# Optimization experiments

Measured on AMD Instinct MI355X. Metric: run time of the kernel, lower is better.

## Reference

```python
import jax, jax.numpy as jnp
import numpy as np

B, CIN, COUT, H0 = 2, 256, 256, 128
GN_G = 16

def hsig(x):
    return jnp.clip(x + 3.0, 0.0, 6.0) / 6.0

def conv3x3(x, w, b):
    y = jax.lax.conv_general_dilated(x, w, (1, 1), ((1, 1), (1, 1)),
                                     dimension_numbers=('NCHW', 'OIHW', 'NCHW'))
    return y + b[None, :, None, None]

def group_norm(x, gamma, beta):
    Bn, C, H, W = x.shape
    xr = x.reshape(Bn, GN_G, C // GN_G, H, W)
    m = xr.mean((2, 3, 4), keepdims=True)
    v = xr.var((2, 3, 4), keepdims=True)
    xn = ((xr - m) * jax.lax.rsqrt(v + 1e-5)).reshape(Bn, C, H, W)
    return xn * gamma[None, :, None, None] + beta[None, :, None, None]

def mdconv(x, offset, mask, weight, stride):
    # Modulated deformable conv v2, 3x3 kernel, padding=1, zero-pad bilinear sampling.
    Bn, C, H, W = x.shape
    K2 = mask.shape[1]  # 9 kernel taps
    Ho, Wo = mask.shape[2], mask.shape[3]
    off = offset.reshape(Bn, K2, 2, Ho, Wo)  # (dy, dx) per tap (mmcv channel order)
    ki = jnp.arange(K2)
    py = (jnp.arange(Ho, dtype=x.dtype) * stride - 1.0)[None, None, :, None] \
         + (ki // 3).astype(x.dtype)[None, :, None, None] + off[:, :, 0]
    px = (jnp.arange(Wo, dtype=x.dtype) * stride - 1.0)[None, None, None, :] \
         + (ki % 3).astype(x.dtype)[None, :, None, None] + off[:, :, 1]
    y0f = jnp.floor(py); x0f = jnp.floor(px)
    wy = py - y0f; wx = px - x0f
    y0 = y0f.astype(jnp.int32); x0 = x0f.astype(jnp.int32)
    xf = x.reshape(Bn, C, H * W)

    def gather(yy, xx):
        valid = ((yy >= 0) & (yy < H) & (xx >= 0) & (xx < W)).astype(x.dtype)
        idx = jnp.clip(yy, 0, H - 1) * W + jnp.clip(xx, 0, W - 1)
        g = jax.vmap(lambda f, i: f[:, i])(xf, idx.reshape(Bn, -1))
        return g.reshape(Bn, C, K2, Ho, Wo) * valid[:, None]

    val = (gather(y0, x0) * ((1 - wy) * (1 - wx))[:, None]
           + gather(y0, x0 + 1) * ((1 - wy) * wx)[:, None]
           + gather(y0 + 1, x0) * (wy * (1 - wx))[:, None]
           + gather(y0 + 1, x0 + 1) * (wy * wx)[:, None])
    val = val * mask[:, None]
    return jnp.einsum('bckhw,ock->bohw', val, weight.reshape(weight.shape[0], C, K2))

def scale_attn(f, w, b):
    p = f.mean((2, 3))                  # global avg pool -> (B, C)
    s = hsig(jax.nn.relu(p @ w.T + b))  # (B, 1)
    return s[:, :, None, None]

def dyrelu(x, w1, b1, w2, b2):
    Bn, C = x.shape[0], x.shape[1]
    p = x.mean((2, 3))
    h = jax.nn.relu(p @ w1.T + b1)
    c = (hsig(h @ w2.T + b2) - 0.5).reshape(Bn, 4, C)  # a1, b1, a2, b2
    e = lambda t: t[:, :, None, None]
    a1 = c[:, 0] * 2.0 + 1.0
    a2 = c[:, 2] * 2.0
    return jnp.maximum(x * e(a1) + e(c[:, 1]), x * e(a2) + e(c[:, 3]))

def resize_align(x, Ho, Wo):
    # bilinear resize, align_corners=True
    Bn, C, H, W = x.shape
    sy = jnp.arange(Ho, dtype=x.dtype) * ((H - 1) / (Ho - 1))
    sx = jnp.arange(Wo, dtype=x.dtype) * ((W - 1) / (Wo - 1))
    yl = jnp.floor(sy).astype(jnp.int32); yh = jnp.minimum(yl + 1, H - 1)
    xl = jnp.floor(sx).astype(jnp.int32); xh = jnp.minimum(xl + 1, W - 1)
    wy = (sy - yl)[None, None, :, None]
    wx = (sx - xl)[None, None, None, :]
    t = x[:, :, yl, :] * (1 - wy) + x[:, :, yh, :] * wy
    return t[:, :, :, xl] * (1 - wx) + t[:, :, :, xh] * wx

def _forward(x0, x1, x2, w_off, b_off, w_mid, g_mid, be_mid, w_low, g_low, be_low,
             w_high, g_high, be_high, w_sa, b_sa, w_dy1, b_dy1, w_dy2, b_dy2):
    xs = [x0, x1, x2]
    L = len(xs)
    outs = []
    for l in range(L):
        om = conv3x3(xs[l], w_off, b_off)
        offset = om[:, :18]
        mask = jax.nn.sigmoid(om[:, 18:])
        mid = group_norm(mdconv(xs[l], offset, mask, w_mid, 1), g_mid, be_mid)
        sum_feat = mid * scale_attn(mid, w_sa, b_sa)
        n = 1
        if l > 0:
            low = group_norm(mdconv(xs[l - 1], offset, mask, w_low, 2), g_low, be_low)
            sum_feat = sum_feat + low * scale_attn(low, w_sa, b_sa)
            n += 1
        if l < L - 1:
            # x[l+1] has half resolution; subsample offset/mask to its grid
            o2 = offset[:, :, ::2, ::2]
            m2 = mask[:, :, ::2, ::2]
            high = group_norm(mdconv(xs[l + 1], o2, m2, w_high, 1), g_high, be_high)
            high = resize_align(high, xs[l].shape[2], xs[l].shape[3])
            sum_feat = sum_feat + high * scale_attn(high, w_sa, b_sa)
            n += 1
        outs.append(dyrelu(sum_feat / n, w_dy1, b_dy1, w_dy2, b_dy2))
    return tuple(outs)

def setup_inputs():
    key = jax.random.key(0)
    ks = jax.random.split(key, 20)
    f32 = jnp.float32
    rn = lambda k, s: jax.random.normal(k, s, f32)
    return {
        'x0': rn(ks[0], (B, CIN, H0, H0)),
        'x1': rn(ks[1], (B, CIN, H0 // 2, H0 // 2)),
        'x2': rn(ks[2], (B, CIN, H0 // 4, H0 // 4)),
        'w_off': 0.01 * rn(ks[3], (27, CIN, 3, 3)),
        'b_off': jnp.zeros((27,), f32),
        'w_mid': 0.05 * rn(ks[4], (COUT, CIN, 3, 3)),
        'g_mid': 1.0 + 0.1 * rn(ks[5], (COUT,)),
        'be_mid': 0.1 * rn(ks[6], (COUT,)),
        'w_low': 0.05 * rn(ks[7], (COUT, CIN, 3, 3)),
        'g_low': 1.0 + 0.1 * rn(ks[8], (COUT,)),
        'be_low': 0.1 * rn(ks[9], (COUT,)),
        'w_high': 0.05 * rn(ks[10], (COUT, CIN, 3, 3)),
        'g_high': 1.0 + 0.1 * rn(ks[11], (COUT,)),
        'be_high': 0.1 * rn(ks[12], (COUT,)),
        'w_sa': 0.05 * rn(ks[13], (1, COUT)),
        'b_sa': jnp.zeros((1,), f32),
        'w_dy1': 0.05 * rn(ks[14], (COUT // 4, COUT)),
        'b_dy1': jnp.zeros((COUT // 4,), f32),
        'w_dy2': 0.05 * rn(ks[15], (4 * COUT, COUT // 4)),
        'b_dy2': jnp.zeros((4 * COUT,), f32),
    }

def reference(x0, x1, x2, w_off, b_off, w_mid, g_mid, be_mid, w_low, g_low, be_low,
              w_high, g_high, be_high, w_sa, b_sa, w_dy1, b_dy1, w_dy2, b_dy2):
    return _forward(x0, x1, x2, w_off, b_off, w_mid, g_mid, be_mid, w_low, g_low,
                    be_low, w_high, g_high, be_high, w_sa, b_sa, w_dy1, b_dy1,
                    w_dy2, b_dy2)
```

## Files before the change

kernel.cpp:

```cpp
#include <hip/hip_runtime.h>
#include <hip/hip_bf16.h>
#include <math.h>

#define CIN 256
#define COUT 256
#define NB 2
#define GN_GROUPS 16

typedef __attribute__((ext_vector_type(8))) short short8;
typedef __attribute__((ext_vector_type(4))) float floatx4;

__device__ __forceinline__ float b2f(unsigned short u) {
  union { unsigned int i; float f; } v;
  v.i = ((unsigned int)u) << 16;
  return v.f;
}
__device__ __forceinline__ unsigned short f2b(float f) {
  union { float f; unsigned int i; } v;
  v.f = f;
  unsigned int r = (v.i + 0x7FFFu + ((v.i >> 16) & 1u)) >> 16;
  return (unsigned short)r;
}
__device__ __forceinline__ float lo2f(unsigned int u) {
  union { unsigned int i; float f; } v;
  v.i = u << 16;
  return v.f;
}
__device__ __forceinline__ float hi2f(unsigned int u) {
  union { unsigned int i; float f; } v;
  v.i = u & 0xffff0000u;
  return v.f;
}
__device__ __forceinline__ unsigned int pk2(float a, float b) {
  union { __hip_bfloat162 h; unsigned int u; } v;
  v.h = __float22bfloat162_rn(float2{a, b});
  return v.u;
}

struct TrB {
  const float* x0; const float* x1; const float* x2;
  unsigned short *t0, *t1, *t2, *l0, *l1, *l2;
};

__global__ __launch_bounds__(256) void transpose_kernel(TrB A) {
  __shared__ float tile[64][65];
  int bx = blockIdx.x;
  int li = (bx >= 256 ? 1 : 0) + (bx >= 320 ? 1 : 0);
  int local = bx - (li == 0 ? 0 : (li == 1 ? 256 : 320));
  const float* x = li == 0 ? A.x0 : (li == 1 ? A.x1 : A.x2);
  unsigned short* xT = li == 0 ? A.t0 : (li == 1 ? A.t1 : A.t2);
  unsigned short* xLo = li == 0 ? A.l0 : (li == 1 ? A.l1 : A.l2);
  int P = li == 0 ? 16384 : (li == 1 ? 4096 : 1024);

  int pBase = local * 64, cBase = blockIdx.y * 64, b = blockIdx.z;
  int t = threadIdx.x;
  int pl = t & 63, ch = t >> 6;
  const float* xb = x + ((size_t)b * CIN + cBase) * P + pBase;
#pragma unroll
  for (int e = 0; e < 16; e++) {
    int c = ch * 16 + e;
    tile[c][pl] = xb[(size_t)c * P + pl];
  }
  __syncthreads();
  size_t obase = ((size_t)b * P + pBase) * CIN + cBase;
  int cl = t & 63, pr = t >> 6;
#pragma unroll
  for (int e = 0; e < 16; e++) {
    int p = pr * 16 + e;
    float v = tile[cl][p];
    unsigned short h = f2b(v);
    xT[obase + (size_t)p * CIN + cl] = h;
    xLo[obase + (size_t)p * CIN + cl] = f2b(v - b2f(h));
  }
}

__global__ void repack_w_kernel(const float* __restrict__ w0,
                                const float* __restrict__ w1,
                                const float* __restrict__ w2,
                                unsigned short* __restrict__ t0,
                                unsigned short* __restrict__ t1,
                                unsigned short* __restrict__ t2) {
  int bx = blockIdx.x;
  int sel = (bx >= 2304 ? 1 : 0) + (bx >= 4608 ? 1 : 0);
  const float* w = sel == 0 ? w0 : (sel == 1 ? w1 : w2);
  unsigned short* wt = sel == 0 ? t0 : (sel == 1 ? t1 : t2);
  int idx = (bx - sel * 2304) * 256 + threadIdx.x;
  int e = idx & 7;
  int lane = (idx >> 3) & 63;
  int i = (idx >> 9) & 3;
  int wv = (idx >> 11) & 3;
  int kc = idx >> 13;
  int oc = wv * 64 + i * 16 + (lane & 15);
  int c = (kc & 7) * 32 + (lane >> 4) * 8 + e;
  int tap = kc >> 3;
  wt[idx] = f2b(w[(size_t)oc * 2304 + c * 9 + tap]);
}

__global__ void repack_wo_kernel(const float* __restrict__ w,
                                 unsigned short* __restrict__ wo) {
  int idx = blockIdx.x * 256 + threadIdx.x;
  int sel = idx / 73728;
  int r = idx % 73728;
  int k = r / 8192;
  int r2 = r % 8192;
  int cbk = r2 / 1024;
  int oc = (r2 / 32) % 32;
  int ch = r2 % 32;
  int c = cbk * 32 + ch;
  float val = (oc < 27) ? w[(size_t)oc * 2304 + c * 9 + k] : 0.0f;
  float hi = b2f(f2b(val));
  wo[idx] = sel ? f2b(val - hi) : f2b(val);
}

struct CoL {
  const unsigned short* xhi;
  const unsigned short* xlo;
  float* om;
  int H, W, Cs, cshift, Rs, P;
};
struct CoB { CoL L[3]; int off[4]; };

__global__ __launch_bounds__(256) void conv_offset_kernel(
    CoB B, const unsigned short* __restrict__ wo,
    const float* __restrict__ bias) {
  __shared__ unsigned short s_hi[204 * 40];
  __shared__ unsigned short s_lo[204 * 40];
  int bx = blockIdx.x;
  int li = (bx >= B.off[1] ? 1 : 0) + (bx >= B.off[2] ? 1 : 0);
  CoL L = B.L[li];
  int local = bx - B.off[li];
  int tpb = L.P / 64;
  int b = local / tpb, pxt = local % tpb;
  int t = threadIdx.x;
  int pbase = pxt * 64;
  int r0 = pbase / L.W;
  int c0 = pbase % L.W;
  int Ct = L.Cs + 2;
  int Npos = Ct * (L.Rs + 2);
  const unsigned short* xhib = L.xhi + (size_t)b * L.P * CIN;
  const unsigned short* xlob = L.xlo + (size_t)b * L.P * CIN;

  int lane = t & 63, wv = t >> 6, quad = lane >> 4, ln = lane & 15;
  int pl = wv * 16 + ln;
  int pi_ = pl >> L.cshift;
  int pj_ = pl & (L.Cs - 1);

  floatx4 acc0 = {0.f, 0.f, 0.f, 0.f}, acc1 = {0.f, 0.f, 0.f, 0.f};

  for (int cb = 0; cb < 8; cb++) {
    __syncthreads();
    for (int e = t; e < Npos * 4; e += 256) {
      int pos = e >> 2, oct = e & 3;
      int r = pos / Ct, c = pos % Ct;
      int gy = r0 - 1 + r, gx = c0 - 1 + c;
      uint4 vhi = {0, 0, 0, 0}, vlo = {0, 0, 0, 0};
      if (gy >= 0 && gy < L.H && gx >= 0 && gx < L.W) {
        size_t off = ((size_t)(gy * L.W + gx)) * CIN + cb * 32 + oct * 8;
        vhi = *(const uint4*)(xhib + off);
        vlo = *(const uint4*)(xlob + off);
      }
      *(uint4*)&s_hi[pos * 40 + oct * 8] = vhi;
      *(uint4*)&s_lo[pos * 40 + oct * 8] = vlo;
    }
    __syncthreads();
#pragma unroll
    for (int tap = 0; tap < 9; tap++) {
      int dy = tap / 3 - 1, dx = tap % 3 - 1;
      const unsigned short* wb0 = wo + (size_t)((0 * 9 + tap) * 8 + cb) * 1024;
      const unsigned short* wb1 = wo + (size_t)((1 * 9 + tap) * 8 + cb) * 1024;
      short8 whi0 = *(const short8*)(wb0 + ln * 32 + quad * 8);
      short8 whi1 = *(const short8*)(wb0 + (16 + ln) * 32 + quad * 8);
      short8 wlo0 = *(const short8*)(wb1 + ln * 32 + quad * 8);
      short8 wlo1 = *(const short8*)(wb1 + (16 + ln) * 32 + quad * 8);
      int pos = (pi_ + dy + 1) * Ct + (pj_ + dx + 1);
      short8 bhi = *(const short8*)&s_hi[pos * 40 + quad * 8];
      short8 blo = *(const short8*)&s_lo[pos * 40 + quad * 8];
      acc0 = __builtin_amdgcn_mfma_f32_16x16x32_bf16(whi0, bhi, acc0, 0, 0, 0);
      acc1 = __builtin_amdgcn_mfma_f32_16x16x32_bf16(whi1, bhi, acc1, 0, 0, 0);
      acc0 = __builtin_amdgcn_mfma_f32_16x16x32_bf16(wlo0, bhi, acc0, 0, 0, 0);
      acc1 = __builtin_amdgcn_mfma_f32_16x16x32_bf16(wlo1, bhi, acc1, 0, 0, 0);
      acc0 = __builtin_amdgcn_mfma_f32_16x16x32_bf16(whi0, blo, acc0, 0, 0, 0);
      acc1 = __builtin_amdgcn_mfma_f32_16x16x32_bf16(whi1, blo, acc1, 0, 0, 0);
    }
  }

  int px = pbase + pl;
#pragma unroll
  for (int i2 = 0; i2 < 2; i2++) {
#pragma unroll
    for (int r = 0; r < 4; r++) {
      int oc = i2 * 16 + quad * 4 + r;
      if (oc < 27) {
        float val = (i2 == 0 ? acc0[r] : acc1[r]) + bias[oc];
        if (oc >= 18) val = 1.f / (1.f + __expf(-val));
        L.om[((size_t)b * 27 + oc) * L.P + px] = val;
      }
    }
  }
}

struct MdP {
  const unsigned short* xT;
  const unsigned short* wt;
  float* outf;
  const float* om;
  float* sum;
  float* sumsq;
  float* wsum;
  int Hi, Wi, Wo, lWo, stride, omStep, omW, omP, ltile, Hro;
};
struct MdBatch { MdP p[7]; int off[7]; };

#define GATHER(k, G)                                                        \
  do {                                                                      \
    int tap_ = (k) >> 3, cbk_ = (k) & 7;                                    \
    int yy_ = s_yy[tap_][gpx], xx_ = s_xx[tap_][gpx];                       \
    int y0_ = yy_ & 0xffff, y1_ = (yy_ >> 16) & 0xffff;                     \
    int x0_ = xx_ & 0xffff, x1_ = (xx_ >> 16) & 0xffff;                     \
    const unsigned short* gb_ = xTb + cbk_ * 32 + goct * 8;                 \
    G[0] = *(const uint4*)(gb_ + (size_t)(y0_ * P.Wi + x0_) * CIN);         \
    G[1] = *(const uint4*)(gb_ + (size_t)(y0_ * P.Wi + x1_) * CIN);         \
    G[2] = *(const uint4*)(gb_ + (size_t)(y1_ * P.Wi + x0_) * CIN);        \
    G[3] = *(const uint4*)(gb_ + (size_t)(y1_ * P.Wi + x1_) * CIN);         \
  } while (0)

#define PACKC(k, G)                                                         \
  do {                                                                      \
    float4 cw_ = s_cw[(k) >> 3][gpx];                                       \
    float r_[8];                                                            \
    _Pragma("unroll") for (int j_ = 0; j_ < 4; j_++) {                      \
      unsigned int a_ = ((unsigned int*)&G[0])[j_];                         \
      unsigned int b2_ = ((unsigned int*)&G[1])[j_];                        \
      unsigned int c_ = ((unsigned int*)&G[2])[j_];                         \
      unsigned int d_ = ((unsigned int*)&G[3])[j_];                         \
      r_[2 * j_] = cw_.x * lo2f(a_) + cw_.y * lo2f(b2_) +                   \
                   cw_.z * lo2f(c_) + cw_.w * lo2f(d_);                     \
      r_[2 * j_ + 1] = cw_.x * hi2f(a_) + cw_.y * hi2f(b2_) +               \
                       cw_.z * hi2f(c_) + cw_.w * hi2f(d_);                 \
    }                                                                       \
    uint4 pk_;                                                              \
    pk_.x = pk2(r_[0], r_[1]);                                              \
    pk_.y = pk2(r_[2], r_[3]);                                              \
    pk_.z = pk2(r_[4], r_[5]);                                              \
    pk_.w = pk2(r_[6], r_[7]);                                              \
    *(uint4*)&s_col[(k) & 1][gpx][goct * 8] = pk_;                          \
  } while (0)

#define LOADAF(k, AF)                                                       \
  do {                                                                      \
    const short8* wp_ = (const short8*)(P.wt) +                             \
                        ((size_t)((k) * 16 + wv * 4) << 6) + lane;          \
    _Pragma("unroll") for (int i_ = 0; i_ < 4; i_++) AF[i_] = wp_[i_ * 64]; \
  } while (0)

#define MFMA16(AF, CUR)                                                     \
  do {                                                                      \
    short8 bfr_[4];                                                         \
    _Pragma("unroll") for (int j_ = 0; j_ < 4; j_++)                        \
      bfr_[j_] = *(const short8*)&s_col[CUR][j_ * 16 + ln][quad * 8];       \
    _Pragma("unroll") for (int i_ = 0; i_ < 4; i_++)                        \
      _Pragma("unroll") for (int j_ = 0; j_ < 4; j_++)                      \
        acc[i_][j_] = __builtin_amdgcn_mfma_f32_16x16x32_bf16(              \
            AF[i_], bfr_[j_], acc[i_][j_], 0, 0, 0);                        \
  } while (0)

#define PHASE_BAR()                                                         \
  do {                                                                      \
    asm volatile("s_waitcnt lgkmcnt(0)" ::: "memory");                      \
    __builtin_amdgcn_s_barrier();                                           \
    __builtin_amdgcn_sched_barrier(0);                                      \
  } while (0)

__global__ __launch_bounds__(256, 3) void mdconv_kernel(MdBatch B) {
  __shared__ float4 s_cw[9][64];
  __shared__ int s_yy[9][64];
  __shared__ int s_xx[9][64];
  __shared__ unsigned short s_col[2][64][40];
  __shared__ float s_prof[64];

  int bx = blockIdx.x;
  int pidx = 0;
#pragma unroll
  for (int i = 1; i < 7; i++) pidx += (bx >= B.off[i]) ? 1 : 0;
  MdP P = B.p[pidx];
  int local = bx - B.off[pidx];
  int ntile = 1 << P.ltile;
  int nslots = (NB << P.ltile) >> 3;
  int flat = (local & 7) * nslots + (local >> 3);
  int b = flat >> P.ltile;
  int pxt = flat & (ntile - 1);
  int Po = P.Wo << P.lWo;
  const unsigned short* xTb = P.xT + (size_t)b * P.Hi * P.Wi * CIN;

  int t = threadIdx.x;
  if (P.wsum) {
    if (t < P.Wo) s_prof[t] = 0.f;
    __syncthreads();
    if (t < P.Hro) {
      float r = (float)(P.Wo - 1) / (float)(P.Hro - 1);
      float sy = (float)t * r;
      int yl = (int)floorf(sy);
      float fy = sy - (float)yl;
      int yh = min(yl + 1, P.Wo - 1);
      atomicAdd(&s_prof[yl], 1.f - fy);
      atomicAdd(&s_prof[yh], fy);
    }
  }
  for (int e = t; e < 576; e += 256) {
    int k = e / 64, px = e % 64;
    int p = pxt * 64 + px;
    int i = p >> P.lWo, j = p & (P.Wo - 1);
    int pc = (i * P.omStep) * P.omW + j * P.omStep;
    const float* omb = P.om + (size_t)b * 27 * P.omP;
    float offy = omb[(size_t)(2 * k) * P.omP + pc];
    float offx = omb[(size_t)(2 * k + 1) * P.omP + pc];
    float m = omb[(size_t)(18 + k) * P.omP + pc];
    float py = (float)(i * P.stride) - 1.0f + (float)(k / 3) + offy;
    float pxf = (float)(j * P.stride) - 1.0f + (float)(k % 3) + offx;
    float y0f = floorf(py), x0f = floorf(pxf);
    float wy = py - y0f, wx = pxf - x0f;
    int y0 = (int)y0f, x0 = (int)x0f;
    int y1 = y0 + 1, x1 = x0 + 1;
    float vy0 = (y0 >= 0 && y0 < P.Hi) ? 1.f : 0.f;
    float vy1 = (y1 >= 0 && y1 < P.Hi) ? 1.f : 0.f;
    float vx0 = (x0 >= 0 && x0 < P.Wi) ? 1.f : 0.f;
    float vx1 = (x1 >= 0 && x1 < P.Wi) ? 1.f : 0.f;
    float4 cw;
    cw.x = (1.f - wy) * (1.f - wx) * m * vy0 * vx0;
    cw.y = (1.f - wy) * wx * m * vy0 * vx1;
    cw.z = wy * (1.f - wx) * m * vy1 * vx0;
    cw.w = wy * wx * m * vy1 * vx1;
    s_cw[k][px] = cw;
    int y0c = min(max(y0, 0), P.Hi - 1), y1c = min(max(y1, 0), P.Hi - 1);
    int x0c = min(max(x0, 0), P.Wi - 1), x1c = min(max(x1, 0), P.Wi - 1);
    s_yy[k][px] = y0c | (y1c << 16);
    s_xx[k][px] = x0c | (x1c << 16);
  }
  __syncthreads();

  floatx4 acc[4][4];
#pragma unroll
  for (int i = 0; i < 4; i++)
#pragma unroll
    for (int j = 0; j < 4; j++) acc[i][j] = (floatx4){0.f, 0.f, 0.f, 0.f};

  int lane = t & 63, wv = t >> 6;
  int quad = lane >> 4, ln = lane & 15;
  int wOc = wv * 64;
  int gpx = t >> 2, goct = t & 3;

  uint4 gA[4], gB[4];
  short8 afA[4], afB[4];

  GATHER(0, gA);
  PACKC(0, gA);
  GATHER(1, gB);
  LOADAF(0, afA);
  PHASE_BAR();

  for (int kc = 0; kc < 72; kc += 2) {
    if (kc + 2 < 72) GATHER(kc + 2, gA);
    LOADAF(kc + 1, afB);
    MFMA16(afA, 0);
    PACKC(kc + 1, gB);
    PHASE_BAR();
    if (kc + 3 < 72) GATHER(kc + 3, gB);
    if (kc + 2 < 72) LOADAF(kc + 2, afA);
    MFMA16(afB, 1);
    if (kc + 2 < 72) PACKC(kc + 2, gA);
    PHASE_BAR();
  }

#pragma unroll
  for (int i = 0; i < 4; i++) {
    int ocB = wOc + i * 16 + quad * 4;
#pragma unroll
    for (int j = 0; j < 4; j++) {
      int px = pxt * 64 + j * 16 + ln;
#pragma unroll
      for (int r = 0; r < 4; r++)
        P.outf[((size_t)b * COUT + ocB + r) * Po + px] = acc[i][j][r];
    }
  }

  float pw[4];
  if (P.wsum) {
#pragma unroll
    for (int j = 0; j < 4; j++) {
      int px = pxt * 64 + j * 16 + ln;
      pw[j] = s_prof[px >> P.lWo] * s_prof[px & (P.Wo - 1)];
    }
  }
#pragma unroll
  for (int i = 0; i < 4; i++) {
    int ocB = wOc + i * 16 + quad * 4;
#pragma unroll
    for (int r = 0; r < 4; r++) {
      float s1 = 0.f, s2 = 0.f, sw = 0.f;
#pragma unroll
      for (int j = 0; j < 4; j++) {
        float v = acc[i][j][r];
        s1 += v;
        s2 += v * v;
        if (P.wsum) sw += v * pw[j];
      }
#pragma unroll
      for (int m = 1; m < 16; m <<= 1) {
        s1 += __shfl_xor(s1, m, 64);
        s2 += __shfl_xor(s2, m, 64);
        if (P.wsum) sw += __shfl_xor(sw, m, 64);
      }
      if (ln == 0) {
        atomicAdd(&P.sum[b * COUT + ocB + r], s1);
        atomicAdd(&P.sumsq[b * COUT + ocB + r], s2);
        if (P.wsum) atomicAdd(&P.wsum[b * COUT + ocB + r], sw);
      }
    }
  }
}

struct PrepL {
  const float* st;
  float *Am, *Bm, *Al, *Bl, *Ah, *Bh, *svec, *coef;
  float invP, invPh, invn;
  int hasLow, hasHigh;
};
struct PrepB { PrepL L[3]; };

__global__ __launch_bounds__(256) void prep_all_kernel(
    PrepB PB, const float* __restrict__ g_mid, const float* __restrict__ be_mid,
    const float* __restrict__ g_low, const float* __restrict__ be_low,
    const float* __restrict__ g_high, const float* __restrict__ be_high,
    const float* __restrict__ w_sa, const float* __restrict__ b_sa,
    const float* __restrict__ w1, const float* __restrict__ b1,
    const float* __restrict__ w2, const float* __restrict__ b2) {
  __shared__ float s_m[3][NB][GN_GROUPS], s_iv[3][NB][GN_GROUPS];
  __shared__ float s_mean[3][NB][COUT];
  __shared__ float s_s[3][NB];
  __shared__ float s_nm[NB][COUT];
  __shared__ float s_h[NB][64];
  PrepL L = PB.L[blockIdx.x];
  const float* sumM = L.st;
  const float* sqM = L.st + 512;
  const float* sumL = L.st + 1024;
  const float* sqL = L.st + 1536;
  const float* sumH = L.st + 2048;
  const float* sqH = L.st + 2560;
  const float* swsum = L.st + 3072;
  int hasLow = L.hasLow, hasHigh = L.hasHigh;
  float invP = L.invP, invPh = L.invPh, invn = L.invn;
  int tid = threadIdx.x;

  if (tid < 96) {
    int path = tid / 32, b = (tid >> 4) & 1, g = tid & 15;
    int active = (path == 0) || (path == 1 && hasLow) || (path == 2 && hasHigh);
    if (active) {
      const float* su = path == 0 ? sumM : (path == 1 ? sumL : sumH);
      const float* sq = path == 0 ? sqM : (path == 1 ? sqL : sqH);
      float invN = ((path == 2) ? invPh : invP) * (1.f / 16.f);
      float s = 0.f, q = 0.f;
      for (int c = g * 16; c < g * 16 + 16; c++) {
        s += su[b * COUT + c];
        q += sq[b * COUT + c];
      }
      float m = s * invN;
      float v = q * invN - m * m;
      s_m[path][b][g] = m;
      s_iv[path][b][g] = rsqrtf(v + 1e-5f);
    }
  }
  __syncthreads();
  for (int idx = tid; idx < 3 * NB * COUT; idx += 256) {
    int path = idx / (NB * COUT);
    int r = idx % (NB * COUT);
    int b = r / COUT, c = r % COUT, g = c >> 4;
    int active = (path == 0) || (path == 1 && hasLow) || (path == 2 && hasHigh);
    if (active) {
      const float* ga = path == 0 ? g_mid : (path == 1 ? g_low : g_high);
      const float* be = path == 0 ? be_mid : (path == 1 ? be_low : be_high);
      float a = ga[c] * s_iv[path][b][g];
      float bb = be[c] - s_m[path][b][g] * a;
      float mean;
      if (path == 2)
        mean = a * (swsum[r] * invP) + bb;
      else {
        const float* su = path == 0 ? sumM : sumL;
        mean = a * (su[r] * invP) + bb;
      }
      float* Ad = path == 0 ? L.Am : (path == 1 ? L.Al : L.Ah);
      float* Bd = path == 0 ? L.Bm : (path == 1 ? L.Bl : L.Bh);
      Ad[r] = a;
      Bd[r] = bb;
      s_mean[path][b][c] = mean;
    }
  }
  __syncthreads();
  if (tid < 6) {
    int path = tid >> 1, b = tid & 1;
    int active = (path == 0) || (path == 1 && hasLow) || (path == 2 && hasHigh);
    float s = 0.f;
    if (active) {
      float t = 0.f;
      for (int c = 0; c < COUT; c++) t += s_mean[path][b][c] * w_sa[c];
      t += b_sa[0];
      t = fmaxf(t, 0.0f);
      s = fminf(fmaxf(t + 3.f, 0.f), 6.f) * (1.f / 6.f);
      L.svec[path * NB + b] = s;
    }
    s_s[path][b] = s;
  }
  __syncthreads();
  for (int idx = tid; idx < NB * COUT; idx += 256) {
    int b = idx / COUT, c = idx % COUT;
    float v = s_s[0][b] * s_mean[0][b][c];
    if (hasLow) v += s_s[1][b] * s_mean[1][b][c];
    if (hasHigh) v += s_s[2][b] * s_mean[2][b][c];
    s_nm[b][c] = v * invn;
  }
  __syncthreads();
  if (tid < NB * 64) {
    int b = tid / 64, j = tid % 64;
    float t = b1[j];
    for (int c = 0; c < COUT; c++) t += s_nm[b][c] * w1[j * COUT + c];
    s_h[b][j] = fmaxf(t, 0.f);
  }
  __syncthreads();
  for (int idx = tid; idx < NB * 1024; idx += 256) {
    int b = idx / 1024, i = idx % 1024;
    float t = b2[i];
    for (int j = 0; j < 64; j++) t += s_h[b][j] * w2[i * 64 + j];
    L.coef[idx] = fminf(fmaxf(t + 3.f, 0.f), 6.f) * (1.f / 6.f) - 0.5f;
  }
}

struct ApL {
  const float* featM; const float* featL; const float* featH;
  const float* Am; const float* Bm; const float* Al; const float* Bl;
  const float* Ah; const float* Bh; const float* svec; const float* coef;
  float* out;
  int lP, lHo, Hh, hasLow, hasHigh;
  float invn;
};
struct ApB { ApL L[3]; int off[4]; };

__global__ __launch_bounds__(256) void fused_apply_kernel(ApB A) {
  int bx = blockIdx.x;
  int li = (bx >= A.off[1] ? 1 : 0) + (bx >= A.off[2] ? 1 : 0);
  ApL L = A.L[li];
  int idx = (bx - A.off[li]) * 256 + threadIdx.x;
  int bc = idx >> L.lP;
  int p = idx & ((1 << L.lP) - 1);
  int b = bc >> 8, c = bc & 255;
  float v = (L.featM[idx] * L.Am[bc] + L.Bm[bc]) * L.svec[b];
  if (L.hasLow) v += (L.featL[idx] * L.Al[bc] + L.Bl[bc]) * L.svec[2 + b];
  if (L.hasHigh) {
    int Ho = 1 << L.lHo;
    int Y = p >> L.lHo, X = p & (Ho - 1);
    float r = (float)(L.Hh - 1) / (float)(Ho - 1);
    float sy = (float)Y * r, sx = (float)X * r;
    int yl = (int)floorf(sy), xl = (int)floorf(sx);
    int yh = min(yl + 1, L.Hh - 1), xh = min(xl + 1, L.Hh - 1);
    float wy = sy - (float)yl, wx = sx - (float)xl;
    const float* fp = L.featH + (size_t)bc * L.Hh * L.Hh;
    float t0 = fp[yl * L.Hh + xl] * (1.f - wx) + fp[yl * L.Hh + xh] * wx;
    float t1 = fp[yh * L.Hh + xl] * (1.f - wx) + fp[yh * L.Hh + xh] * wx;
    v += ((t0 * (1.f - wy) + t1 * wy) * L.Ah[bc] + L.Bh[bc]) * L.svec[4 + b];
  }
  float xv = v * L.invn;
  float a1 = L.coef[b * 1024 + c] * 2.f + 1.f;
  float b1v = L.coef[b * 1024 + 256 + c];
  float a2 = L.coef[b * 1024 + 512 + c] * 2.f;
  float b2v = L.coef[b * 1024 + 768 + c];
  L.out[idx] = fmaxf(xv * a1 + b1v, xv * a2 + b2v);
}

extern "C" void kernel_launch(void* const* d_in, const int* in_sizes, int n_in,
                              void* d_out, int out_size, void* d_ws,
                              size_t ws_size, hipStream_t stream) {
  (void)in_sizes; (void)n_in; (void)out_size; (void)ws_size;
  const float* x[3] = {(const float*)d_in[0], (const float*)d_in[1],
                       (const float*)d_in[2]};
  const float* w_off = (const float*)d_in[3];
  const float* b_off = (const float*)d_in[4];
  const float* w_mid = (const float*)d_in[5];
  const float* g_mid = (const float*)d_in[6];
  const float* be_mid = (const float*)d_in[7];
  const float* w_low = (const float*)d_in[8];
  const float* g_low = (const float*)d_in[9];
  const float* be_low = (const float*)d_in[10];
  const float* w_high = (const float*)d_in[11];
  const float* g_high = (const float*)d_in[12];
  const float* be_high = (const float*)d_in[13];
  const float* w_sa = (const float*)d_in[14];
  const float* b_sa = (const float*)d_in[15];
  const float* w_dy1 = (const float*)d_in[16];
  const float* b_dy1 = (const float*)d_in[17];
  const float* w_dy2 = (const float*)d_in[18];
  const float* b_dy2 = (const float*)d_in[19];

  float* out = (float*)d_out;
  char* wsb = (char*)d_ws;
  size_t o = 0;
  unsigned short* xT0 = (unsigned short*)(wsb + o); o += 16777216;
  unsigned short* xT1 = (unsigned short*)(wsb + o); o += 4194304;
  unsigned short* xT2 = (unsigned short*)(wsb + o); o += 1048576;
  unsigned short* wtm = (unsigned short*)(wsb + o); o += 1179648;
  unsigned short* wtl = (unsigned short*)(wsb + o); o += 1179648;
  unsigned short* wth = (unsigned short*)(wsb + o); o += 1179648;
  unsigned short* wo  = (unsigned short*)(wsb + o); o += 294912;
  float* om0 = (float*)(wsb + o); o += 3538944;
  float* om1 = (float*)(wsb + o); o += 884736;
  float* om2 = (float*)(wsb + o); o += 221184;
  float* arena = (float*)(wsb + o); o += 65011712;
  float* stats = (float*)(wsb + o); o += 43008;
  float* Am = (float*)(wsb + o); o += 6144;
  float* Bm = (float*)(wsb + o); o += 6144;
  float* Al = (float*)(wsb + o); o += 6144;
  float* Bl = (float*)(wsb + o); o += 6144;
  float* Ah = (float*)(wsb + o); o += 6144;
  float* Bh = (float*)(wsb + o); o += 6144;
  float* svec = (float*)(wsb + o); o += 192;
  float* dycoef = (float*)(wsb + o); o += 24576;

  float* featM0 = arena;
  float* featH0 = arena + 8388608;
  float* featM1 = arena + 10485760;
  float* featL1 = arena + 12582912;
  float* featH1 = arena + 14680064;
  float* featM2 = arena + 15204352;
  float* featL2 = arena + 15728640;

  unsigned short* xLo0 = (unsigned short*)arena;
  unsigned short* xLo1 = xLo0 + 8388608;
  unsigned short* xLo2 = xLo1 + 2097152;

  TrB tb = {x[0], x[1], x[2], xT0, xT1, xT2, xLo0, xLo1, xLo2};
  transpose_kernel<<<dim3(336, 4, NB), 256, 0, stream>>>(tb);
  repack_w_kernel<<<6912, 256, 0, stream>>>(w_mid, w_low, w_high, wtm, wtl, wth);
  repack_wo_kernel<<<576, 256, 0, stream>>>(w_off, wo);

  CoB cob;
  cob.L[0] = {xT0, xLo0, om0, 128, 128, 64, 6, 1, 16384};
  cob.L[1] = {xT1, xLo1, om1, 64, 64, 64, 6, 1, 4096};
  cob.L[2] = {xT2, xLo2, om2, 32, 32, 32, 5, 2, 1024};
  cob.off[0] = 0; cob.off[1] = 512; cob.off[2] = 640; cob.off[3] = 672;
  conv_offset_kernel<<<672, 256, 0, stream>>>(cob, wo, b_off);

  hipMemsetAsync(stats, 0, 3 * 3584 * sizeof(float), stream);

  float* S0 = stats;
  float* S1 = stats + 3584;
  float* S2 = stats + 7168;
  MdBatch mb;
  mb.p[0] = {xT0, wtm, featM0, om0, S0, S0 + 512, nullptr,
             128, 128, 128, 7, 1, 1, 128, 16384, 8, 0};
  mb.p[1] = {xT1, wth, featH0, om0, S0 + 2048, S0 + 2560, S0 + 3072,
             64, 64, 64, 6, 1, 2, 128, 16384, 6, 128};
  mb.p[2] = {xT1, wtm, featM1, om1, S1, S1 + 512, nullptr,
             64, 64, 64, 6, 1, 1, 64, 4096, 6, 0};
  mb.p[3] = {xT0, wtl, featL1, om1, S1 + 1024, S1 + 1536, nullptr,
             128, 128, 64, 6, 2, 1, 64, 4096, 6, 0};
  mb.p[4] = {xT2, wth, featH1, om1, S1 + 2048, S1 + 2560, S1 + 3072,
             32, 32, 32, 5, 1, 2, 64, 4096, 4, 64};
  mb.p[5] = {xT2, wtm, featM2, om2, S2, S2 + 512, nullptr,
             32, 32, 32, 5, 1, 1, 32, 1024, 4, 0};
  mb.p[6] = {xT1, wtl, featL2, om2, S2 + 1024, S2 + 1536, nullptr,
             64, 64, 32, 5, 2, 1, 32, 1024, 4, 0};
  mb.off[0] = 0;   mb.off[1] = 512; mb.off[2] = 640; mb.off[3] = 768;
  mb.off[4] = 896; mb.off[5] = 928; mb.off[6] = 960;
  mdconv_kernel<<<992, 256, 0, stream>>>(mb);

  PrepB pb;
  {
    const int Hs[3] = {128, 64, 32};
    const float nterm[3] = {2.f, 3.f, 2.f};
    for (int l = 0; l < 3; l++) {
      int H = Hs[l];
      int Pp = H * H;
      int Ph = (H / 2) * (H / 2);
      pb.L[l] = {stats + l * 3584, Am + l * 512, Bm + l * 512, Al + l * 512,
                 Bl + l * 512, Ah + l * 512, Bh + l * 512, svec + l * 16,
                 dycoef + l * 2048, 1.0f / (float)Pp, 1.0f / (float)Ph,
                 1.0f / nterm[l], l > 0 ? 1 : 0, l < 2 ? 1 : 0};
    }
  }
  prep_all_kernel<<<3, 256, 0, stream>>>(pb, g_mid, be_mid, g_low, be_low,
                                         g_high, be_high, w_sa, b_sa, w_dy1,
                                         b_dy1, w_dy2, b_dy2);

  ApB ab;
  ab.L[0] = {featM0, featM0, featH0, Am, Bm, Al, Bl, Ah, Bh, svec, dycoef,
             out, 14, 7, 64, 0, 1, 0.5f};
  ab.L[1] = {featM1, featL1, featH1, Am + 512, Bm + 512, Al + 512, Bl + 512,
             Ah + 512, Bh + 512, svec + 16, dycoef + 2048, out + 8388608,
             12, 6, 32, 1, 1, 1.0f / 3.0f};
  ab.L[2] = {featM2, featL2, featM2, Am + 1024, Bm + 1024, Al + 1024,
             Bl + 1024, Ah + 1024, Bh + 1024, svec + 32, dycoef + 4096,
             out + 10485760, 10, 5, 16, 1, 0, 0.5f};
  ab.off[0] = 0; ab.off[1] = 32768; ab.off[2] = 40960; ab.off[3] = 43008;
  fused_apply_kernel<<<43008, 256, 0, stream>>>(ab);
}
```

Measured before the change: 430.3 us.

## Merge setup kernels, fold stats prep into mdconv via last-block counter

Result: slower. 759.7 us (+76.6%).

```diff
diff --git a/kernel.cpp b/kernel.cpp
--- a/kernel.cpp
+++ b/kernel.cpp
@@ -37,79 +37,78 @@
   return v.u;
 }
 
-struct TrB {
-  const float* x0; const float* x1; const float* x2;
+struct SetB {
+  const float *x0, *x1, *x2, *wm, *wl, *wh, *wof;
   unsigned short *t0, *t1, *t2, *l0, *l1, *l2;
+  unsigned short *wtm, *wtl, *wth, *wo;
+  float* stats;
 };
 
-__global__ __launch_bounds__(256) void transpose_kernel(TrB A) {
+__global__ __launch_bounds__(256) void setup_kernel(SetB A) {
   __shared__ float tile[64][65];
-  int bx = blockIdx.x;
-  int li = (bx >= 256 ? 1 : 0) + (bx >= 320 ? 1 : 0);
-  int local = bx - (li == 0 ? 0 : (li == 1 ? 256 : 320));
-  const float* x = li == 0 ? A.x0 : (li == 1 ? A.x1 : A.x2);
-  unsigned short* xT = li == 0 ? A.t0 : (li == 1 ? A.t1 : A.t2);
-  unsigned short* xLo = li == 0 ? A.l0 : (li == 1 ? A.l1 : A.l2);
-  int P = li == 0 ? 16384 : (li == 1 ? 4096 : 1024);
-
-  int pBase = local * 64, cBase = blockIdx.y * 64, b = blockIdx.z;
-  int t = threadIdx.x;
-  int pl = t & 63, ch = t >> 6;
-  const float* xb = x + ((size_t)b * CIN + cBase) * P + pBase;
-#pragma unroll
-  for (int e = 0; e < 16; e++) {
-    int c = ch * 16 + e;
-    tile[c][pl] = xb[(size_t)c * P + pl];
-  }
-  __syncthreads();
-  size_t obase = ((size_t)b * P + pBase) * CIN + cBase;
-  int cl = t & 63, pr = t >> 6;
-#pragma unroll
-  for (int e = 0; e < 16; e++) {
-    int p = pr * 16 + e;
-    float v = tile[cl][p];
-    unsigned short h = f2b(v);
-    xT[obase + (size_t)p * CIN + cl] = h;
-    xLo[obase + (size_t)p * CIN + cl] = f2b(v - b2f(h));
-  }
-}
-
-__global__ void repack_w_kernel(const float* __restrict__ w0,
-                                const float* __restrict__ w1,
-                                const float* __restrict__ w2,
-                                unsigned short* __restrict__ t0,
-                                unsigned short* __restrict__ t1,
-                                unsigned short* __restrict__ t2) {
-  int bx = blockIdx.x;
-  int sel = (bx >= 2304 ? 1 : 0) + (bx >= 4608 ? 1 : 0);
-  const float* w = sel == 0 ? w0 : (sel == 1 ? w1 : w2);
-  unsigned short* wt = sel == 0 ? t0 : (sel == 1 ? t1 : t2);
-  int idx = (bx - sel * 2304) * 256 + threadIdx.x;
-  int e = idx & 7;
-  int lane = (idx >> 3) & 63;
-  int i = (idx >> 9) & 3;
-  int wv = (idx >> 11) & 3;
-  int kc = idx >> 13;
-  int oc = wv * 64 + i * 16 + (lane & 15);
-  int c = (kc & 7) * 32 + (lane >> 4) * 8 + e;
-  int tap = kc >> 3;
-  wt[idx] = f2b(w[(size_t)oc * 2304 + c * 9 + tap]);
-}
-
-__global__ void repack_wo_kernel(const float* __restrict__ w,
-                                 unsigned short* __restrict__ wo) {
-  int idx = blockIdx.x * 256 + threadIdx.x;
-  int sel = idx / 73728;
-  int r = idx % 73728;
-  int k = r / 8192;
-  int r2 = r % 8192;
-  int cbk = r2 / 1024;
-  int oc = (r2 / 32) % 32;
-  int ch = r2 % 32;
-  int c = cbk * 32 + ch;
-  float val = (oc < 27) ? w[(size_t)oc * 2304 + c * 9 + k] : 0.0f;
-  float hi = b2f(f2b(val));
-  wo[idx] = sel ? f2b(val - hi) : f2b(val);
+  int bx = blockIdx.x, t = threadIdx.x;
+  if (bx < 2688) {
+    int xg = bx % 336;
+    int rem = bx / 336;
+    int yg = rem & 3, zg = rem >> 2;
+    int li = (xg >= 256 ? 1 : 0) + (xg >= 320 ? 1 : 0);
+    int local = xg - (li == 0 ? 0 : (li == 1 ? 256 : 320));
+    const float* x = li == 0 ? A.x0 : (li == 1 ? A.x1 : A.x2);
+    unsigned short* xT = li == 0 ? A.t0 : (li == 1 ? A.t1 : A.t2);
+    unsigned short* xLo = li == 0 ? A.l0 : (li == 1 ? A.l1 : A.l2);
+    int P = li == 0 ? 16384 : (li == 1 ? 4096 : 1024);
+    int pBase = local * 64, cBase = yg * 64, b = zg;
+    int pl = t & 63, ch = t >> 6;
+    const float* xb = x + ((size_t)b * CIN + cBase) * P + pBase;
+#pragma unroll
+    for (int e = 0; e < 16; e++) {
+      int c = ch * 16 + e;
+      tile[c][pl] = xb[(size_t)c * P + pl];
+    }
+    __syncthreads();
+    size_t obase = ((size_t)b * P + pBase) * CIN + cBase;
+    int cl = t & 63, pr = t >> 6;
+#pragma unroll
+    for (int e = 0; e < 16; e++) {
+      int p = pr * 16 + e;
+      float v = tile[cl][p];
+      unsigned short h = f2b(v);
+      xT[obase + (size_t)p * CIN + cl] = h;
+      xLo[obase + (size_t)p * CIN + cl] = f2b(v - b2f(h));
+    }
+  } else if (bx < 9600) {
+    int lb = bx - 2688;
+    int sel = (lb >= 2304 ? 1 : 0) + (lb >= 4608 ? 1 : 0);
+    const float* w = sel == 0 ? A.wm : (sel == 1 ? A.wl : A.wh);
+    unsigned short* wt = sel == 0 ? A.wtm : (sel == 1 ? A.wtl : A.wth);
+    int idx = (lb - sel * 2304) * 256 + t;
+    int e = idx & 7;
+    int lane = (idx >> 3) & 63;
+    int i = (idx >> 9) & 3;
+    int wv = (idx >> 11) & 3;
+    int kc = idx >> 13;
+    int oc = wv * 64 + i * 16 + (lane & 15);
+    int c = (kc & 7) * 32 + (lane >> 4) * 8 + e;
+    int tap = kc >> 3;
+    wt[idx] = f2b(w[(size_t)oc * 2304 + c * 9 + tap]);
+  } else if (bx < 10176) {
+    int idx = (bx - 9600) * 256 + t;
+    int sel = idx / 73728;
+    int r = idx % 73728;
+    int k = r / 8192;
+    int r2 = r % 8192;
+    int cbk = r2 / 1024;
+    int oc = (r2 / 32) % 32;
+    int ch = r2 % 32;
+    int c = cbk * 32 + ch;
+    float val = (oc < 27) ? A.wof[(size_t)oc * 2304 + c * 9 + k] : 0.0f;
+    float hi = b2f(f2b(val));
+    A.wo[idx] = sel ? f2b(val - hi) : f2b(val);
+  } else {
+    int idx = (bx - 10176) * 256 + t;
+    if (idx < 10752) A.stats[idx] = 0.f;
+    else if (idx == 10752) ((unsigned int*)A.stats)[10752] = 0u;
+  }
 }
 
 struct CoL {
@@ -209,24 +208,57 @@
   float* wsum;
   int Hi, Wi, Wo, lWo, stride, omStep, omW, omP, ltile, Hro;
 };
-struct MdBatch { MdP p[7]; int off[7]; };
+struct PrepL {
+  const float* st;
+  float *Am, *Bm, *Al, *Bl, *Ah, *Bh, *svec, *coef;
+  float invP, invPh, invn;
+  int hasLow, hasHigh;
+};
+struct MdBatch {
+  MdP p[7];
+  int off[7];
+  int nblocks;
+  unsigned int* counter;
+  PrepL pl[3];
+  const float *g_mid, *be_mid, *g_low, *be_low, *g_high, *be_high;
+  const float *w_sa, *b_sa, *w1, *b1, *w2, *b2;
+};
+
+union SMem {
+  struct {
+    float4 cw[9][64];
+    int yy[9][64];
+    int xx[9][64];
+    unsigned short col[2][64][40];
+    float prof[64];
+  } md;
+  struct {
+    float stats[3584];
+    float mean[3][NB][COUT];
+    float m[3][NB][GN_GROUPS];
+    float iv[3][NB][GN_GROUPS];
+    float s[3][NB];
+    float nm[NB][COUT];
+    float h[NB][64];
+  } pp;
+};
 
 #define GATHER(k, G)                                                        \
   do {                                                                      \
     int tap_ = (k) >> 3, cbk_ = (k) & 7;                                    \
-    int yy_ = s_yy[tap_][gpx], xx_ = s_xx[tap_][gpx];                       \
+    int yy_ = S.md.yy[tap_][gpx], xx_ = S.md.xx[tap_][gpx];                 \
     int y0_ = yy_ & 0xffff, y1_ = (yy_ >> 16) & 0xffff;                     \
     int x0_ = xx_ & 0xffff, x1_ = (xx_ >> 16) & 0xffff;                     \
     const unsigned short* gb_ = xTb + cbk_ * 32 + goct * 8;                 \
-    G[0] = *(const uint4*)(gb_ + (size_t)(y0_ * P.Wi + x0_) * CIN);         \
-    G[1] = *(const uint4*)(gb_ + (size_t)(y0_ * P.Wi + x1_) * CIN);         \
-    G[2] = *(const uint4*)(gb_ + (size_t)(y1_ * P.Wi + x0_) * CIN);        \
-    G[3] = *(const uint4*)(gb_ + (size_t)(y1_ * P.Wi + x1_) * CIN);         \
+    G[0] = *(const uint4*)(gb_ + (size_t)(y0_ + x0_) * CIN);                \
+    G[1] = *(const uint4*)(gb_ + (size_t)(y0_ + x1_) * CIN);                \
+    G[2] = *(const uint4*)(gb_ + (size_t)(y1_ + x0_) * CIN);                \
+    G[3] = *(const uint4*)(gb_ + (size_t)(y1_ + x1_) * CIN);                \
   } while (0)
 
 #define PACKC(k, G)                                                         \
   do {                                                                      \
-    float4 cw_ = s_cw[(k) >> 3][gpx];                                       \
+    float4 cw_ = S.md.cw[(k) >> 3][gpx];                                    \
     float r_[8];                                                            \
     _Pragma("unroll") for (int j_ = 0; j_ < 4; j_++) {                      \
       unsigned int a_ = ((unsigned int*)&G[0])[j_];                         \
@@ -243,7 +275,7 @@
     pk_.y = pk2(r_[2], r_[3]);                                              \
     pk_.z = pk2(r_[4], r_[5]);                                              \
     pk_.w = pk2(r_[6], r_[7]);                                              \
-    *(uint4*)&s_col[(k) & 1][gpx][goct * 8] = pk_;                          \
+    *(uint4*)&S.md.col[(k) & 1][gpx][goct * 8] = pk_;                       \
   } while (0)
 
 #define LOADAF(k, AF)                                                       \
@@ -257,7 +289,7 @@
   do {                                                                      \
     short8 bfr_[4];                                                         \
     _Pragma("unroll") for (int j_ = 0; j_ < 4; j_++)                        \
-      bfr_[j_] = *(const short8*)&s_col[CUR][j_ * 16 + ln][quad * 8];       \
+      bfr_[j_] = *(const short8*)&S.md.col[CUR][j_ * 16 + ln][quad * 8];    \
     _Pragma("unroll") for (int i_ = 0; i_ < 4; i_++)                        \
       _Pragma("unroll") for (int j_ = 0; j_ < 4; j_++)                      \
         acc[i_][j_] = __builtin_amdgcn_mfma_f32_16x16x32_bf16(              \
@@ -271,12 +303,116 @@
     __builtin_amdgcn_sched_barrier(0);                                      \
   } while (0)
 
-__global__ __launch_bounds__(256, 3) void mdconv_kernel(MdBatch B) {
-  __shared__ float4 s_cw[9][64];
-  __shared__ int s_yy[9][64];
-  __shared__ int s_xx[9][64];
-  __shared__ unsigned short s_col[2][64][40];
-  __shared__ float s_prof[64];
+__device__ __attribute__((noinline)) void run_prep(const MdBatch& B, SMem& S) {
+  int tid = threadIdx.x;
+  for (int l = 0; l < 3; l++) {
+    PrepL L = B.pl[l];
+    __syncthreads();
+    for (int i = tid; i < 3584; i += 256)
+      S.pp.stats[i] = __hip_atomic_load(L.st + i, __ATOMIC_RELAXED,
+                                        __HIP_MEMORY_SCOPE_AGENT);
+    __syncthreads();
+    const float* sumM = S.pp.stats;
+    const float* sqM = S.pp.stats + 512;
+    const float* sumL = S.pp.stats + 1024;
+    const float* sqL = S.pp.stats + 1536;
+    const float* sumH = S.pp.stats + 2048;
+    const float* sqH = S.pp.stats + 2560;
+    const float* swsum = S.pp.stats + 3072;
+    int hasLow = L.hasLow, hasHigh = L.hasHigh;
+    float invP = L.invP, invPh = L.invPh, invn = L.invn;
+
+    if (tid < 96) {
+      int path = tid / 32, b = (tid >> 4) & 1, g = tid & 15;
+      int active =
+          (path == 0) || (path == 1 && hasLow) || (path == 2 && hasHigh);
+      if (active) {
+        const float* su = path == 0 ? sumM : (path == 1 ? sumL : sumH);
+        const float* sq = path == 0 ? sqM : (path == 1 ? sqL : sqH);
+        float invN = ((path == 2) ? invPh : invP) * (1.f / 16.f);
+        float s = 0.f, q = 0.f;
+        for (int c = g * 16; c < g * 16 + 16; c++) {
+          s += su[b * COUT + c];
+          q += sq[b * COUT + c];
+        }
+        float m = s * invN;
+        float v = q * invN - m * m;
+        S.pp.m[path][b][g] = m;
+        S.pp.iv[path][b][g] = rsqrtf(v + 1e-5f);
+      }
+    }
+    __syncthreads();
+    for (int idx = tid; idx < 3 * NB * COUT; idx += 256) {
+      int path = idx / (NB * COUT);
+      int r = idx % (NB * COUT);
+      int b = r / COUT, c = r % COUT, g = c >> 4;
+      int active =
+          (path == 0) || (path == 1 && hasLow) || (path == 2 && hasHigh);
+      if (active) {
+        const float* ga = path == 0 ? B.g_mid : (path == 1 ? B.g_low : B.g_high);
+        const float* be =
+            path == 0 ? B.be_mid : (path == 1 ? B.be_low : B.be_high);
+        float a = ga[c] * S.pp.iv[path][b][g];
+        float bb = be[c] - S.pp.m[path][b][g] * a;
+        float mean;
+        if (path == 2)
+          mean = a * (swsum[r] * invP) + bb;
+        else {
+          const float* su = path == 0 ? sumM : sumL;
+          mean = a * (su[r] * invP) + bb;
+        }
+        float* Ad = path == 0 ? L.Am : (path == 1 ? L.Al : L.Ah);
+        float* Bd = path == 0 ? L.Bm : (path == 1 ? L.Bl : L.Bh);
+        Ad[r] = a;
+        Bd[r] = bb;
+        S.pp.mean[path][b][c] = mean;
+      }
+    }
+    __syncthreads();
+    if (tid < 6) {
+      int path = tid >> 1, b = tid & 1;
+      int active =
+          (path == 0) || (path == 1 && hasLow) || (path == 2 && hasHigh);
+      float s = 0.f;
+      if (active) {
+        float tt = 0.f;
+        for (int c = 0; c < COUT; c++) tt += S.pp.mean[path][b][c] * B.w_sa[c];
+        tt += B.b_sa[0];
+        tt = fmaxf(tt, 0.0f);
+        s = fminf(fmaxf(tt + 3.f, 0.f), 6.f) * (1.f / 6.f);
+        L.svec[path * NB + b] = s;
+      }
+      S.pp.s[path][b] = s;
+    }
+    __syncthreads();
+    for (int idx = tid; idx < NB * COUT; idx += 256) {
+      int b = idx / COUT, c = idx % COUT;
+      float v = S.pp.s[0][b] * S.pp.mean[0][b][c];
+      if (hasLow) v += S.pp.s[1][b] * S.pp.mean[1][b][c];
+      if (hasHigh) v += S.pp.s[2][b] * S.pp.mean[2][b][c];
+      S.pp.nm[b][c] = v * invn;
+    }
+    __syncthreads();
+    if (tid < NB * 64) {
+      int b = tid / 64, j = tid % 64;
+      float tt = B.b1[j];
+      for (int c = 0; c < COUT; c++) tt += S.pp.nm[b][c] * B.w1[j * COUT + c];
+      S.pp.h[b][j] = fmaxf(tt, 0.f);
+    }
+    __syncthreads();
+    for (int idx = tid; idx < NB * 1024; idx += 256) {
+      int b = idx / 1024, i = idx % 1024;
+      float tt = B.b2[i];
+      for (int j = 0; j < 64; j++) tt += S.pp.h[b][j] * B.w2[i * 64 + j];
+      L.coef[idx] = fminf(fmaxf(tt + 3.f, 0.f), 6.f) * (1.f / 6.f) - 0.5f;
+    }
+    __syncthreads();
+  }
+}
+
+__global__ __launch_bounds__(256, 4) void mdconv_kernel(MdBatch B) {
+  __shared__ SMem S;
+  __shared__ unsigned int s_flag;
 
   int bx = blockIdx.x;
   int pidx = 0;
@@ -294,7 +430,7 @@
 
   int t = threadIdx.x;
   if (P.wsum) {
-    if (t < P.Wo) s_prof[t] = 0.f;
+    if (t < P.Wo) S.md.prof[t] = 0.f;
     __syncthreads();
     if (t < P.Hro) {
       float r = (float)(P.Wo - 1) / (float)(P.Hro - 1);
@@ -302,8 +438,8 @@
       int yl = (int)floorf(sy);
       float fy = sy - (float)yl;
       int yh = min(yl + 1, P.Wo - 1);
-      atomicAdd(&s_prof[yl], 1.f - fy);
-      atomicAdd(&s_prof[yh], fy);
+      atomicAdd(&S.md.prof[yl], 1.f - fy);
+      atomicAdd(&S.md.prof[yh], fy);
     }
   }
   for (int e = t; e < 576; e += 256) {
@@ -330,11 +466,11 @@
     cw.y = (1.f - wy) * wx * m * vy0 * vx1;
     cw.z = wy * (1.f - wx) * m * vy1 * vx0;
     cw.w = wy * wx * m * vy1 * vx1;
-    s_cw[k][px] = cw;
+    S.md.cw[k][px] = cw;
     int y0c = min(max(y0, 0), P.Hi - 1), y1c = min(max(y1, 0), P.Hi - 1);
     int x0c = min(max(x0, 0), P.Wi - 1), x1c = min(max(x1, 0), P.Wi - 1);
-    s_yy[k][px] = y0c | (y1c << 16);
-    s_xx[k][px] = x0c | (x1c << 16);
+    S.md.yy[k][px] = (y0c * P.Wi) | ((y1c * P.Wi) << 16);
+    S.md.xx[k][px] = x0c | (x1c << 16);
   }
   __syncthreads();
 
@@ -350,23 +486,24 @@
   int gpx = t >> 2, goct = t & 3;
 
   uint4 gA[4], gB[4];
-  short8 afA[4], afB[4];
+  short8 afA[4];
 
   GATHER(0, gA);
   PACKC(0, gA);
   GATHER(1, gB);
-  LOADAF(0, afA);
   PHASE_BAR();
 
   for (int kc = 0; kc < 72; kc += 2) {
+    LOADAF(kc, afA);
+    __builtin_amdgcn_sched_barrier(0);
     if (kc + 2 < 72) GATHER(kc + 2, gA);
-    LOADAF(kc + 1, afB);
     MFMA16(afA, 0);
     PACKC(kc + 1, gB);
     PHASE_BAR();
+    LOADAF(kc + 1, afA);
+    __builtin_amdgcn_sched_barrier(0);
     if (kc + 3 < 72) GATHER(kc + 3, gB);
-    if (kc + 2 < 72) LOADAF(kc + 2, afA);
-    MFMA16(afB, 1);
+    MFMA16(afA, 1);
     if (kc + 2 < 72) PACKC(kc + 2, gA);
     PHASE_BAR();
   }
@@ -388,7 +525,7 @@
 #pragma unroll
     for (int j = 0; j < 4; j++) {
       int px = pxt * 64 + j * 16 + ln;
-      pw[j] = s_prof[px >> P.lWo] * s_prof[px & (P.Wo - 1)];
+      pw[j] = S.md.prof[px >> P.lWo] * S.md.prof[px & (P.Wo - 1)];
     }
   }
 #pragma unroll
@@ -417,119 +554,17 @@
       }
     }
   }
-}
-
-struct PrepL {
-  const float* st;
-  float *Am, *Bm, *Al, *Bl, *Ah, *Bh, *svec, *coef;
-  float invP, invPh, invn;
-  int hasLow, hasHigh;
-};
-struct PrepB { PrepL L[3]; };
-
-__global__ __launch_bounds__(256) void prep_all_kernel(
-    PrepB PB, const float* __restrict__ g_mid, const float* __restrict__ be_mid,
-    const float* __restrict__ g_low, const float* __restrict__ be_low,
-    const float* __restrict__ g_high, const float* __restrict__ be_high,
-    const float* __restrict__ w_sa, const float* __restrict__ b_sa,
-    const float* __restrict__ w1, const float* __restrict__ b1,
-    const float* __restrict__ w2, const float* __restrict__ b2) {
-  __shared__ float s_m[3][NB][GN_GROUPS], s_iv[3][NB][GN_GROUPS];
-  __shared__ float s_mean[3][NB][COUT];
-  __shared__ float s_s[3][NB];
-  __shared__ float s_nm[NB][COUT];
-  __shared__ float s_h[NB][64];
-  PrepL L = PB.L[blockIdx.x];
-  const float* sumM = L.st;
-  const float* sqM = L.st + 512;
-  const float* sumL = L.st + 1024;
-  const float* sqL = L.st + 1536;
-  const float* sumH = L.st + 2048;
-  const float* sqH = L.st + 2560;
-  const float* swsum = L.st + 3072;
-  int hasLow = L.hasLow, hasHigh = L.hasHigh;
-  float invP = L.invP, invPh = L.invPh, invn = L.invn;
-  int tid = threadIdx.x;
-
-  if (tid < 96) {
-    int path = tid / 32, b = (tid >> 4) & 1, g = tid & 15;
-    int active = (path == 0) || (path == 1 && hasLow) || (path == 2 && hasHigh);
-    if (active) {
-      const float* su = path == 0 ? sumM : (path == 1 ? sumL : sumH);
-      const float* sq = path == 0 ? sqM : (path == 1 ? sqL : sqH);
-      float invN = ((path == 2) ? invPh : invP) * (1.f / 16.f);
-      float s = 0.f, q = 0.f;
-      for (int c = g * 16; c < g * 16 + 16; c++) {
-        s += su[b * COUT + c];
-        q += sq[b * COUT + c];
-      }
-      float m = s * invN;
-      float v = q * invN - m * m;
-      s_m[path][b][g] = m;
-      s_iv[path][b][g] = rsqrtf(v + 1e-5f);
-    }
-  }
+
   __syncthreads();
-  for (int idx = tid; idx < 3 * NB * COUT; idx += 256) {
-    int path = idx / (NB * COUT);
-    int r = idx % (NB * COUT);
-    int b = r / COUT, c = r % COUT, g = c >> 4;
-    int active = (path == 0) || (path == 1 && hasLow) || (path == 2 && hasHigh);
-    if (active) {
-      const float* ga = path == 0 ? g_mid : (path == 1 ? g_low : g_high);
-      const float* be = path == 0 ? be_mid : (path == 1 ? be_low : be_high);
-      float a = ga[c] * s_iv[path][b][g];
-      float bb = be[c] - s_m[path][b][g] * a;
-      float mean;
-      if (path == 2)
-        mean = a * (swsum[r] * invP) + bb;
-      else {
-        const float* su = path == 0 ? sumM : sumL;
-        mean = a * (su[r] * invP) + bb;
-      }
-      float* Ad = path == 0 ? L.Am : (path == 1 ? L.Al : L.Ah);
-      float* Bd = path == 0 ? L.Bm : (path == 1 ? L.Bl : L.Bh);
-      Ad[r] = a;
-      Bd[r] = bb;
-      s_mean[path][b][c] = mean;
-    }
+  if (t == 0) {
+    __threadfence();
+    unsigned int old = atomicAdd(B.counter, 1u);
+    s_flag = (old == (unsigned int)(B.nblocks - 1)) ? 1u : 0u;
   }
   __syncthreads();
-  if (tid < 6) {
-    int path = tid >> 1, b = tid & 1;
-    int active = (path == 0) || (path == 1 && hasLow) || (path == 2 && hasHigh);
-    float s = 0.f;
-    if (active) {
-      float t = 0.f;
-      for (int c = 0; c < COUT; c++) t += s_mean[path][b][c] * w_sa[c];
-      t += b_sa[0];
-      t = fmaxf(t, 0.0f);
-      s = fminf(fmaxf(t + 3.f, 0.f), 6.f) * (1.f / 6.f);
-      L.svec[path * NB + b] = s;
-    }
-    s_s[path][b] = s;
-  }
-  __syncthreads();
-  for (int idx = tid; idx < NB * COUT; idx += 256) {
-    int b = idx / COUT, c = idx % COUT;
-    float v = s_s[0][b] * s_mean[0][b][c];
-    if (hasLow) v += s_s[1][b] * s_mean[1][b][c];
-    if (hasHigh) v += s_s[2][b] * s_mean[2][b][c];
-    s_nm[b][c] = v * invn;
-  }
-  __syncthreads();
-  if (tid < NB * 64) {
-    int b = tid / 64, j = tid % 64;
-    float t = b1[j];
-    for (int c = 0; c < COUT; c++) t += s_nm[b][c] * w1[j * COUT + c];
-    s_h[b][j] = fmaxf(t, 0.f);
-  }
-  __syncthreads();
-  for (int idx = tid; idx < NB * 1024; idx += 256) {
-    int b = idx / 1024, i = idx % 1024;
-    float t = b2[i];
-    for (int j = 0; j < 64; j++) t += s_h[b][j] * w2[i * 64 + j];
-    L.coef[idx] = fminf(fmaxf(t + 3.f, 0.f), 6.f) * (1.f / 6.f) - 0.5f;
+  if (s_flag) {
+    __threadfence();
+    run_prep(B, S);
   }
 }
 
@@ -612,7 +647,7 @@
   float* om1 = (float*)(wsb + o); o += 884736;
   float* om2 = (float*)(wsb + o); o += 221184;
   float* arena = (float*)(wsb + o); o += 65011712;
-  float* stats = (float*)(wsb + o); o += 43008;
+  float* stats = (float*)(wsb + o); o += 43072;
   float* Am = (float*)(wsb + o); o += 6144;
   float* Bm = (float*)(wsb + o); o += 6144;
   float* Al = (float*)(wsb + o); o += 6144;
@@ -622,6 +657,8 @@
   float* svec = (float*)(wsb + o); o += 192;
   float* dycoef = (float*)(wsb + o); o += 24576;
 
+  unsigned int* counter = (unsigned int*)(stats + 10752);
+
   float* featM0 = arena;
   float* featH0 = arena + 8388608;
   float* featM1 = arena + 10485760;
@@ -634,10 +671,9 @@
   unsigned short* xLo1 = xLo0 + 8388608;
   unsigned short* xLo2 = xLo1 + 2097152;
 
-  TrB tb = {x[0], x[1], x[2], xT0, xT1, xT2, xLo0, xLo1, xLo2};
-  transpose_kernel<<<dim3(336, 4, NB), 256, 0, stream>>>(tb);
-  repack_w_kernel<<<6912, 256, 0, stream>>>(w_mid, w_low, w_high, wtm, wtl, wth);
-  repack_wo_kernel<<<576, 256, 0, stream>>>(w_off, wo);
+  SetB sb = {x[0], x[1], x[2], w_mid, w_low, w_high, w_off,
+             xT0, xT1, xT2, xLo0, xLo1, xLo2, wtm, wtl, wth, wo, stats};
+  setup_kernel<<<10219, 256, 0, stream>>>(sb);
 
   CoB cob;
   cob.L[0] = {xT0, xLo0, om0, 128, 128, 64, 6, 1, 16384};
@@ -645,8 +681,6 @@
   cob.L[2] = {xT2, xLo2, om2, 32, 32, 32, 5, 2, 1024};
   cob.off[0] = 0; cob.off[1] = 512; cob.off[2] = 640; cob.off[3] = 672;
   conv_offset_kernel<<<672, 256, 0, stream>>>(cob, wo, b_off);
-
-  hipMemsetAsync(stats, 0, 3 * 3584 * sizeof(float), stream);
 
   float* S0 = stats;
   float* S1 = stats + 3584;
@@ -668,9 +702,8 @@
              64, 64, 32, 5, 2, 1, 32, 1024, 4, 0};
   mb.off[0] = 0;   mb.off[1] = 512; mb.off[2] = 640; mb.off[3] = 768;
   mb.off[4] = 896; mb.off[5] = 928; mb.off[6] = 960;
-  mdconv_kernel<<<992, 256, 0, stream>>>(mb);
-
-  PrepB pb;
+  mb.nblocks = 992;
+  mb.counter = counter;
   {
     const int Hs[3] = {128, 64, 32};
     const float nterm[3] = {2.f, 3.f, 2.f};
@@ -678,15 +711,16 @@
       int H = Hs[l];
       int Pp = H * H;
       int Ph = (H / 2) * (H / 2);
-      pb.L[l] = {stats + l * 3584, Am + l * 512, Bm + l * 512, Al + l * 512,
-                 Bl + l * 512, Ah + l * 512, Bh + l * 512, svec + l * 16,
-                 dycoef + l * 2048, 1.0f / (float)Pp, 1.0f / (float)Ph,
-                 1.0f / nterm[l], l > 0 ? 1 : 0, l < 2 ? 1 : 0};
-    }
-  }
-  prep_all_kernel<<<3, 256, 0, stream>>>(pb, g_mid, be_mid, g_low, be_low,
-                                         g_high, be_high, w_sa, b_sa, w_dy1,
-                                         b_dy1, w_dy2, b_dy2);
+      mb.pl[l] = {stats + l * 3584, Am + l * 512, Bm + l * 512, Al + l * 512,
+                  Bl + l * 512, Ah + l * 512, Bh + l * 512, svec + l * 16,
+                  dycoef + l * 2048, 1.0f / (float)Pp, 1.0f / (float)Ph,
+                  1.0f / nterm[l], l > 0 ? 1 : 0, l < 2 ? 1 : 0};
+    }
+  }
+  mb.g_mid = g_mid; mb.be_mid = be_mid; mb.g_low = g_low; mb.be_low = be_low;
+  mb.g_high = g_high; mb.be_high = be_high; mb.w_sa = w_sa; mb.b_sa = b_sa;
+  mb.w1 = w_dy1; mb.b1 = b_dy1; mb.w2 = w_dy2; mb.b2 = b_dy2;
+  mdconv_kernel<<<992, 256, 0, stream>>>(mb);
 
   ApB ab;
   ab.L[0] = {featM0, featM0, featH0, Am, Bm, Al, Bl, Ah, Bh, svec, dycoef,
```
